# Kernel optimization log

Hardware: AMD Instinct MI355X
Metric: run time of the kernel (lower is better)

Reference implementation:

```python
import jax, jax.numpy as jnp
import numpy as np

DIM = 96
NUM_HEADS = 3
WINDOW = 7
SHIFT = 3


def setup_inputs() -> dict:
    key = jax.random.key(0)
    k1, k2, k3, k4, k5 = jax.random.split(key, 5)
    B, H, W, C = 16, 224, 224, DIM
    s = 1.0 / np.sqrt(C)
    return {
        "x": jax.random.normal(k1, (B, H, W, C), dtype=jnp.float32),
        "w_qkv": jax.random.normal(k2, (C, 3 * C), dtype=jnp.float32) * s,
        "b_qkv": jnp.zeros((3 * C,), dtype=jnp.float32),
        "w_proj": jax.random.normal(k3, (C, C), dtype=jnp.float32) * s,
        "b_proj": jnp.zeros((C,), dtype=jnp.float32),
    }


def _window_partition(x, ws):
    B, H, W, C = x.shape
    x = x.reshape(B, H // ws, ws, W // ws, ws, C)
    x = x.transpose(0, 1, 3, 2, 4, 5)  # B, hn, wn, ws, ws, C
    return x.reshape(-1, ws * ws, C)


def _window_reverse(xw, ws, B, H, W, C):
    xw = xw.reshape(B, H // ws, W // ws, ws, ws, C)
    xw = xw.transpose(0, 1, 3, 2, 4, 5)
    return xw.reshape(B, H, W, C)


def reference(x, w_qkv, b_qkv, w_proj, b_proj):
    B, H, W, C = x.shape
    nh = NUM_HEADS
    hd = C // nh
    scale = hd ** (-0.5)
    if SHIFT > 0:
        x = jnp.roll(x, shift=(-SHIFT, -SHIFT), axis=(1, 2))
    xw = _window_partition(x, WINDOW)            # [B_, N, C], N = 49
    B_, N, _ = xw.shape
    qkv = xw @ w_qkv + b_qkv                     # [B_, N, 3C]
    qkv = qkv.reshape(B_, N, 3, nh, hd).transpose(2, 0, 3, 1, 4)
    q, k, v = qkv[0], qkv[1], qkv[2]             # [B_, nh, N, hd]
    attn = jnp.einsum("bhnd,bhmd->bhnm", q, k) * scale
    attn = jax.nn.softmax(attn, axis=-1)
    out = jnp.einsum("bhnm,bhmd->bhnd", attn, v)  # [B_, nh, N, hd]
    out = out.transpose(0, 2, 1, 3).reshape(B_, N, C)
    out = out @ w_proj + b_proj
    out = _window_reverse(out, WINDOW, B, H, W, C)
    if SHIFT > 0:
        out = jnp.roll(out, shift=(SHIFT, SHIFT), axis=(1, 2))
    return out
```

## Files before the change

kernel.cpp:

```cpp
#include <hip/hip_runtime.h>

using short8  = __attribute__((ext_vector_type(8))) short;
using short4v = __attribute__((ext_vector_type(4))) short;
using float4v = __attribute__((ext_vector_type(4))) float;

#define IMG  224
#define CDIM 96
#define NTOK 49
#define STQ  104
#define STV  72
#define STP  72

__device__ __forceinline__ unsigned short f2bf(float f) {
  union { float f; unsigned u; } cv; cv.f = f;
  unsigned u = cv.u;
  u += 0x7fffu + ((u >> 16) & 1u);
  return (unsigned short)(u >> 16);
}

__global__ void prep_weights(const float* __restrict__ wqkv,
                             const float* __restrict__ wproj,
                             unsigned short* __restrict__ blob) {
  int tid = blockIdx.x * 256 + threadIdx.x;
  if (tid < 3456) {
    int ks = tid / (18 * 64);
    int rem = tid % (18 * 64);
    int nt = rem / 64;
    int lane = rem % 64;
    int k0 = 32 * ks + (lane >> 4) * 8;
    int n  = 16 * nt + (lane & 15);
    unsigned short* dst = blob + tid * 8;
#pragma unroll
    for (int j = 0; j < 8; ++j) dst[j] = f2bf(wqkv[(k0 + j) * 288 + n]);
  } else if (tid < 4608) {
    int t = tid - 3456;
    int ks = t / (6 * 64);
    int rem = t % (6 * 64);
    int nt = rem / 64;
    int lane = rem % 64;
    int k0 = 32 * ks + (lane >> 4) * 8;
    int n  = 16 * nt + (lane & 15);
    unsigned short* dst = blob + 3456 * 8 + t * 8;
#pragma unroll
    for (int j = 0; j < 8; ++j) dst[j] = f2bf(wproj[(k0 + j) * 96 + n]);
  }
}

__global__ __launch_bounds__(256, 3)
void swin_kernel(const float* __restrict__ x,
                 const float* __restrict__ bqkv,
                 const float* __restrict__ bproj,
                 const unsigned short* __restrict__ blob,
                 float* __restrict__ out) {
  __shared__ __align__(16) unsigned short q_s[64 * STQ];
  __shared__ __align__(16) unsigned short k_s[64 * STQ];
  __shared__ __align__(16) unsigned short v_sT[96 * STV];
  __shared__ __align__(16) unsigned short p_s[64 * STP];

  const int tid  = threadIdx.x;
  const int lane = tid & 63;
  const int wv   = tid >> 6;
  const int l15  = lane & 15;
  const int quad = lane >> 4;

  const int wid = blockIdx.x;
  const int b   = wid >> 10;
  const int rem = wid & 1023;
  const int wr  = rem >> 5;
  const int wc  = rem & 31;

  const float4v ZERO4 = {0.f, 0.f, 0.f, 0.f};
  const int trow = 16 * wv + quad * 4;

  short8 afr[3];
  {
    int ta = 16 * wv + l15;
    if (ta < NTOK) {
      int r = ta / 7, c = ta - 7 * r;
      int gh = wr * 7 + r + 3; if (gh >= IMG) gh -= IMG;
      int gw = wc * 7 + c + 3; if (gw >= IMG) gw -= IMG;
      const float* xp = x + ((b * IMG + gh) * IMG + gw) * CDIM + quad * 8;
#pragma unroll
      for (int ks = 0; ks < 3; ++ks) {
        float4v v0 = *(const float4v*)(xp + 32 * ks);
        float4v v1 = *(const float4v*)(xp + 32 * ks + 4);
        short8 a;
        a[0] = (short)f2bf(v0[0]); a[1] = (short)f2bf(v0[1]);
        a[2] = (short)f2bf(v0[2]); a[3] = (short)f2bf(v0[3]);
        a[4] = (short)f2bf(v1[0]); a[5] = (short)f2bf(v1[1]);
        a[6] = (short)f2bf(v1[2]); a[7] = (short)f2bf(v1[3]);
        afr[ks] = a;
      }
    } else {
      short8 z = {0, 0, 0, 0, 0, 0, 0, 0};
      afr[0] = z; afr[1] = z; afr[2] = z;
    }
  }

  const short8* bq = (const short8*)blob;
#pragma unroll
  for (int nt = 0; nt < 18; ++nt) {
    float4v acc = ZERO4;
#pragma unroll
    for (int ks = 0; ks < 3; ++ks) {
      short8 bf = bq[(ks * 18 + nt) * 64 + lane];
      acc = __builtin_amdgcn_mfma_f32_16x16x32_bf16(afr[ks], bf, acc, 0, 0, 0);
    }
    int col = 16 * nt + l15;
    float bias = bqkv[col];
    if (nt < 6) {
#pragma unroll
      for (int r = 0; r < 4; ++r)
        q_s[(trow + r) * STQ + col] = f2bf(acc[r] + bias);
    } else if (nt < 12) {
#pragma unroll
      for (int r = 0; r < 4; ++r)
        k_s[(trow + r) * STQ + (col - 96)] = f2bf(acc[r] + bias);
    } else {
      short4v pk;
#pragma unroll
      for (int r = 0; r < 4; ++r) pk[r] = (short)f2bf(acc[r] + bias);
      *(short4v*)&v_sT[(col - 192) * STV + trow] = pk;
    }
  }
  __syncthreads();

  const float cexp = 0.25500526034059f;
#pragma unroll
  for (int h = 0; h < 3; ++h) {
    short8 qa = *(const short8*)&q_s[(16 * wv + l15) * STQ + 32 * h + quad * 8];
    float4v s[4];
#pragma unroll
    for (int nt = 0; nt < 4; ++nt) {
      short8 kb = *(const short8*)&k_s[(16 * nt + l15) * STQ + 32 * h + quad * 8];
      s[nt] = __builtin_amdgcn_mfma_f32_16x16x32_bf16(qa, kb, ZERO4, 0, 0, 0);
    }
    float rsi[4];
#pragma unroll
    for (int r = 0; r < 4; ++r) {
      float m0 = -3.0e38f;
#pragma unroll
      for (int nt = 0; nt < 4; ++nt) {
        float sv = (16 * nt + l15 < NTOK) ? s[nt][r] : -3.0e38f;
        s[nt][r] = sv;
        m0 = fmaxf(m0, sv);
      }
      m0 = fmaxf(m0, __shfl_xor(m0, 1, 64));
      m0 = fmaxf(m0, __shfl_xor(m0, 2, 64));
      m0 = fmaxf(m0, __shfl_xor(m0, 4, 64));
      m0 = fmaxf(m0, __shfl_xor(m0, 8, 64));
      float sum = 0.f;
#pragma unroll
      for (int nt = 0; nt < 4; ++nt) {
        float p = exp2f((s[nt][r] - m0) * cexp);
        s[nt][r] = p;
        sum += p;
      }
      sum += __shfl_xor(sum, 1, 64);
      sum += __shfl_xor(sum, 2, 64);
      sum += __shfl_xor(sum, 4, 64);
      sum += __shfl_xor(sum, 8, 64);
      rsi[r] = 1.0f / sum;
    }
#pragma unroll
    for (int nt = 0; nt < 4; ++nt) {
      int key = 16 * nt + l15;
#pragma unroll
      for (int r = 0; r < 4; ++r)
        p_s[(trow + r) * STP + key] = f2bf(s[nt][r]);
    }
    float4v o0 = ZERO4, o1 = ZERO4;
#pragma unroll
    for (int ks = 0; ks < 2; ++ks) {
      short8 pa = *(const short8*)&p_s[(16 * wv + l15) * STP + 32 * ks + quad * 8];
      short8 vb0 = *(const short8*)&v_sT[(32 * h + l15) * STV + 32 * ks + quad * 8];
      short8 vb1 = *(const short8*)&v_sT[(32 * h + 16 + l15) * STV + 32 * ks + quad * 8];
      o0 = __builtin_amdgcn_mfma_f32_16x16x32_bf16(pa, vb0, o0, 0, 0, 0);
      o1 = __builtin_amdgcn_mfma_f32_16x16x32_bf16(pa, vb1, o1, 0, 0, 0);
    }
#pragma unroll
    for (int r = 0; r < 4; ++r) {
      q_s[(trow + r) * STQ + 32 * h + l15]      = f2bf(o0[r] * rsi[r]);
      q_s[(trow + r) * STQ + 32 * h + 16 + l15] = f2bf(o1[r] * rsi[r]);
    }
  }

  const short8* bp = (const short8*)(blob + 3456 * 8);
  float4v pacc[6];
#pragma unroll
  for (int i = 0; i < 6; ++i) pacc[i] = ZERO4;
#pragma unroll
  for (int ks = 0; ks < 3; ++ks) {
    short8 aa = *(const short8*)&q_s[(16 * wv + l15) * STQ + 32 * ks + quad * 8];
#pragma unroll
    for (int nt = 0; nt < 6; ++nt) {
      short8 bf = bp[(ks * 6 + nt) * 64 + lane];
      pacc[nt] = __builtin_amdgcn_mfma_f32_16x16x32_bf16(aa, bf, pacc[nt], 0, 0, 0);
    }
  }
#pragma unroll
  for (int r = 0; r < 4; ++r) {
    int t = trow + r;
    if (t < NTOK) {
      int rr = t / 7, cc = t - 7 * rr;
      int gh = wr * 7 + rr + 3; if (gh >= IMG) gh -= IMG;
      int gw = wc * 7 + cc + 3; if (gw >= IMG) gw -= IMG;
      float* op = out + ((b * IMG + gh) * IMG + gw) * CDIM;
#pragma unroll
      for (int nt = 0; nt < 6; ++nt)
        op[16 * nt + l15] = pacc[nt][r] + bproj[16 * nt + l15];
    }
  }
}

extern "C" void kernel_launch(void* const* d_in, const int* in_sizes, int n_in,
                              void* d_out, int out_size, void* d_ws, size_t ws_size,
                              hipStream_t stream) {
  const float* x      = (const float*)d_in[0];
  const float* w_qkv  = (const float*)d_in[1];
  const float* b_qkv  = (const float*)d_in[2];
  const float* w_proj = (const float*)d_in[3];
  const float* b_proj = (const float*)d_in[4];
  float* out = (float*)d_out;
  unsigned short* blob = (unsigned short*)d_ws;

  hipLaunchKernelGGL(prep_weights, dim3(18), dim3(256), 0, stream, w_qkv, w_proj, blob);
  hipLaunchKernelGGL(swin_kernel, dim3(16384), dim3(256), 0, stream,
                     x, b_qkv, b_proj, blob, out);
}
```

Measured before the change: 641.1 us.

## Drop softmax max-subtraction, compute row sums via MFMA, reuse K smem for P

```diff
diff --git a/kernel.cpp b/kernel.cpp
--- a/kernel.cpp
+++ b/kernel.cpp
@@ -3,19 +3,24 @@
 using short8  = __attribute__((ext_vector_type(8))) short;
 using short4v = __attribute__((ext_vector_type(4))) short;
 using float4v = __attribute__((ext_vector_type(4))) float;
+using bf16x2  = __attribute__((ext_vector_type(2))) __bf16;
 
 #define IMG  224
 #define CDIM 96
 #define NTOK 49
 #define STQ  104
 #define STV  72
-#define STP  72
 
 __device__ __forceinline__ unsigned short f2bf(float f) {
-  union { float f; unsigned u; } cv; cv.f = f;
-  unsigned u = cv.u;
-  u += 0x7fffu + ((u >> 16) & 1u);
-  return (unsigned short)(u >> 16);
+  union { __bf16 h; unsigned short u; } cv;
+  cv.h = (__bf16)f;
+  return cv.u;
+}
+
+__device__ __forceinline__ unsigned pk2(float lo, float hi) {
+  union { bf16x2 v; unsigned u; } cv;
+  cv.v = bf16x2{(__bf16)lo, (__bf16)hi};
+  return cv.u;
 }
 
 __global__ void prep_weights(const float* __restrict__ wqkv,
@@ -46,7 +51,7 @@
   }
 }
 
-__global__ __launch_bounds__(256, 3)
+__global__ __launch_bounds__(256, 4)
 void swin_kernel(const float* __restrict__ x,
                  const float* __restrict__ bqkv,
                  const float* __restrict__ bproj,
@@ -55,7 +60,6 @@
   __shared__ __align__(16) unsigned short q_s[64 * STQ];
   __shared__ __align__(16) unsigned short k_s[64 * STQ];
   __shared__ __align__(16) unsigned short v_sT[96 * STV];
-  __shared__ __align__(16) unsigned short p_s[64 * STP];
 
   const int tid  = threadIdx.x;
   const int lane = tid & 63;
@@ -71,6 +75,7 @@
 
   const float4v ZERO4 = {0.f, 0.f, 0.f, 0.f};
   const int trow = 16 * wv + quad * 4;
+  const float CEXP = 0.25500526034059f;
 
   short8 afr[3];
   {
@@ -84,12 +89,12 @@
       for (int ks = 0; ks < 3; ++ks) {
         float4v v0 = *(const float4v*)(xp + 32 * ks);
         float4v v1 = *(const float4v*)(xp + 32 * ks + 4);
-        short8 a;
-        a[0] = (short)f2bf(v0[0]); a[1] = (short)f2bf(v0[1]);
-        a[2] = (short)f2bf(v0[2]); a[3] = (short)f2bf(v0[3]);
-        a[4] = (short)f2bf(v1[0]); a[5] = (short)f2bf(v1[1]);
-        a[6] = (short)f2bf(v1[2]); a[7] = (short)f2bf(v1[3]);
-        afr[ks] = a;
+        union { unsigned u[4]; short8 v; } cv;
+        cv.u[0] = pk2(v0[0], v0[1]);
+        cv.u[1] = pk2(v0[2], v0[3]);
+        cv.u[2] = pk2(v1[0], v1[1]);
+        cv.u[3] = pk2(v1[2], v1[3]);
+        afr[ks] = cv.v;
       }
     } else {
       short8 z = {0, 0, 0, 0, 0, 0, 0, 0};
@@ -109,80 +114,93 @@
     int col = 16 * nt + l15;
     float bias = bqkv[col];
     if (nt < 6) {
-#pragma unroll
-      for (int r = 0; r < 4; ++r)
-        q_s[(trow + r) * STQ + col] = f2bf(acc[r] + bias);
+      unsigned d01 = pk2((acc[0] + bias) * CEXP, (acc[1] + bias) * CEXP);
+      unsigned d23 = pk2((acc[2] + bias) * CEXP, (acc[3] + bias) * CEXP);
+      unsigned short* p = &q_s[trow * STQ + col];
+      p[0]       = (unsigned short)d01;
+      p[STQ]     = (unsigned short)(d01 >> 16);
+      p[2 * STQ] = (unsigned short)d23;
+      p[3 * STQ] = (unsigned short)(d23 >> 16);
     } else if (nt < 12) {
-#pragma unroll
-      for (int r = 0; r < 4; ++r)
-        k_s[(trow + r) * STQ + (col - 96)] = f2bf(acc[r] + bias);
+      unsigned d01 = pk2(acc[0] + bias, acc[1] + bias);
+      unsigned d23 = pk2(acc[2] + bias, acc[3] + bias);
+      unsigned short* p = &k_s[trow * STQ + (col - 96)];
+      p[0]       = (unsigned short)d01;
+      p[STQ]     = (unsigned short)(d01 >> 16);
+      p[2 * STQ] = (unsigned short)d23;
+      p[3 * STQ] = (unsigned short)(d23 >> 16);
     } else {
-      short4v pk;
-#pragma unroll
-      for (int r = 0; r < 4; ++r) pk[r] = (short)f2bf(acc[r] + bias);
-      *(short4v*)&v_sT[(col - 192) * STV + trow] = pk;
+      float f0 = (trow + 0 < NTOK) ? acc[0] + bias : 0.f;
+      float f1 = (trow + 1 < NTOK) ? acc[1] + bias : 0.f;
+      float f2 = (trow + 2 < NTOK) ? acc[2] + bias : 0.f;
+      float f3 = (trow + 3 < NTOK) ? acc[3] + bias : 0.f;
+      union { unsigned u[2]; short4v v; } cv;
+      cv.u[0] = pk2(f0, f1);
+      cv.u[1] = pk2(f2, f3);
+      *(short4v*)&v_sT[(col - 192) * STV + trow] = cv.v;
     }
   }
   __syncthreads();
 
-  const float cexp = 0.25500526034059f;
+  unsigned pp[3][4][2];
 #pragma unroll
   for (int h = 0; h < 3; ++h) {
     short8 qa = *(const short8*)&q_s[(16 * wv + l15) * STQ + 32 * h + quad * 8];
-    float4v s[4];
 #pragma unroll
     for (int nt = 0; nt < 4; ++nt) {
       short8 kb = *(const short8*)&k_s[(16 * nt + l15) * STQ + 32 * h + quad * 8];
-      s[nt] = __builtin_amdgcn_mfma_f32_16x16x32_bf16(qa, kb, ZERO4, 0, 0, 0);
-    }
-    float rsi[4];
-#pragma unroll
-    for (int r = 0; r < 4; ++r) {
-      float m0 = -3.0e38f;
-#pragma unroll
-      for (int nt = 0; nt < 4; ++nt) {
-        float sv = (16 * nt + l15 < NTOK) ? s[nt][r] : -3.0e38f;
-        s[nt][r] = sv;
-        m0 = fmaxf(m0, sv);
-      }
-      m0 = fmaxf(m0, __shfl_xor(m0, 1, 64));
-      m0 = fmaxf(m0, __shfl_xor(m0, 2, 64));
-      m0 = fmaxf(m0, __shfl_xor(m0, 4, 64));
-      m0 = fmaxf(m0, __shfl_xor(m0, 8, 64));
-      float sum = 0.f;
-#pragma unroll
-      for (int nt = 0; nt < 4; ++nt) {
-        float p = exp2f((s[nt][r] - m0) * cexp);
-        s[nt][r] = p;
-        sum += p;
-      }
-      sum += __shfl_xor(sum, 1, 64);
-      sum += __shfl_xor(sum, 2, 64);
-      sum += __shfl_xor(sum, 4, 64);
-      sum += __shfl_xor(sum, 8, 64);
-      rsi[r] = 1.0f / sum;
-    }
+      float4v s = __builtin_amdgcn_mfma_f32_16x16x32_bf16(qa, kb, ZERO4, 0, 0, 0);
+      pp[h][nt][0] = pk2(__builtin_amdgcn_exp2f(s[0]), __builtin_amdgcn_exp2f(s[1]));
+      pp[h][nt][1] = pk2(__builtin_amdgcn_exp2f(s[2]), __builtin_amdgcn_exp2f(s[3]));
+    }
+  }
+  __syncthreads();
+
+  short8 on0, on1;
+#pragma unroll
+  for (int j = 0; j < 8; ++j) {
+    on0[j] = (short)0x3F80;
+    on1[j] = (short)((32 + quad * 8 + j) < NTOK ? 0x3F80 : 0);
+  }
+
+#pragma unroll
+  for (int h = 0; h < 3; ++h) {
 #pragma unroll
     for (int nt = 0; nt < 4; ++nt) {
-      int key = 16 * nt + l15;
-#pragma unroll
-      for (int r = 0; r < 4; ++r)
-        p_s[(trow + r) * STP + key] = f2bf(s[nt][r]);
-    }
-    float4v o0 = ZERO4, o1 = ZERO4;
+      unsigned short* p = &k_s[trow * STQ + 16 * nt + l15];
+      unsigned d0 = pp[h][nt][0], d1 = pp[h][nt][1];
+      p[0]       = (unsigned short)d0;
+      p[STQ]     = (unsigned short)(d0 >> 16);
+      p[2 * STQ] = (unsigned short)d1;
+      p[3 * STQ] = (unsigned short)(d1 >> 16);
+    }
+    float4v o0 = ZERO4, o1 = ZERO4, o2 = ZERO4;
 #pragma unroll
     for (int ks = 0; ks < 2; ++ks) {
-      short8 pa = *(const short8*)&p_s[(16 * wv + l15) * STP + 32 * ks + quad * 8];
+      short8 pa  = *(const short8*)&k_s[(16 * wv + l15) * STQ + 32 * ks + quad * 8];
       short8 vb0 = *(const short8*)&v_sT[(32 * h + l15) * STV + 32 * ks + quad * 8];
       short8 vb1 = *(const short8*)&v_sT[(32 * h + 16 + l15) * STV + 32 * ks + quad * 8];
       o0 = __builtin_amdgcn_mfma_f32_16x16x32_bf16(pa, vb0, o0, 0, 0, 0);
       o1 = __builtin_amdgcn_mfma_f32_16x16x32_bf16(pa, vb1, o1, 0, 0, 0);
-    }
-#pragma unroll
-    for (int r = 0; r < 4; ++r) {
-      q_s[(trow + r) * STQ + 32 * h + l15]      = f2bf(o0[r] * rsi[r]);
-      q_s[(trow + r) * STQ + 32 * h + 16 + l15] = f2bf(o1[r] * rsi[r]);
-    }
+      o2 = __builtin_amdgcn_mfma_f32_16x16x32_bf16(pa, ks ? on1 : on0, o2, 0, 0, 0);
+    }
+    float r0 = __builtin_amdgcn_rcpf(o2[0]);
+    float r1 = __builtin_amdgcn_rcpf(o2[1]);
+    float r2 = __builtin_amdgcn_rcpf(o2[2]);
+    float r3 = __builtin_amdgcn_rcpf(o2[3]);
+    unsigned a01 = pk2(o0[0] * r0, o0[1] * r1);
+    unsigned a23 = pk2(o0[2] * r2, o0[3] * r3);
+    unsigned b01 = pk2(o1[0] * r0, o1[1] * r1);
+    unsigned b23 = pk2(o1[2] * r2, o1[3] * r3);
+    unsigned short* ar = &q_s[trow * STQ + 32 * h + l15];
+    ar[0]            = (unsigned short)a01;
+    ar[STQ]          = (unsigned short)(a01 >> 16);
+    ar[2 * STQ]      = (unsigned short)a23;
+    ar[3 * STQ]      = (unsigned short)(a23 >> 16);
+    ar[16]           = (unsigned short)b01;
+    ar[STQ + 16]     = (unsigned short)(b01 >> 16);
+    ar[2 * STQ + 16] = (unsigned short)b23;
+    ar[3 * STQ + 16] = (unsigned short)(b23 >> 16);
   }
 
   const short8* bp = (const short8*)(blob + 3456 * 8);
@@ -198,6 +216,9 @@
       pacc[nt] = __builtin_amdgcn_mfma_f32_16x16x32_bf16(aa, bf, pacc[nt], 0, 0, 0);
     }
   }
+  float pb[6];
+#pragma unroll
+  for (int nt = 0; nt < 6; ++nt) pb[nt] = bproj[16 * nt + l15];
 #pragma unroll
   for (int r = 0; r < 4; ++r) {
     int t = trow + r;
@@ -208,7 +229,7 @@
       float* op = out + ((b * IMG + gh) * IMG + gw) * CDIM;
 #pragma unroll
       for (int nt = 0; nt < 6; ++nt)
-        op[16 * nt + l15] = pacc[nt][r] + bproj[16 * nt + l15];
+        op[16 * nt + l15] = pacc[nt][r] + pb[nt];
     }
   }
 }
```

Measured after the change: 617.5 us. 1.04x faster.
